# Optimization experiments

Hardware: AMD Instinct MI355X
Metric: run time of the kernel (lower is better)

Reference implementation:

```python
import jax, jax.numpy as jnp
import numpy as np
from jax import lax

B, C, T = 64, 122, 500
COUT, D, H, FF, L = 64, 128, 8, 256, 2
NSUB, NCLS = 13, 4
EPS = 1e-5


def _gelu(x):
    return jax.nn.gelu(x, approximate=False)  # torch nn.GELU default (erf)


def _bn(x, g, b, m, v):
    # eval-mode BatchNorm1d over channel dim of [N, C, T]
    scale = (g / jnp.sqrt(v + EPS))[None, :, None]
    return (x - m[None, :, None]) * scale + b[None, :, None]


def _ln(x, g, b):
    mu = x.mean(-1, keepdims=True)
    var = ((x - mu) ** 2).mean(-1, keepdims=True)
    return (x - mu) / jnp.sqrt(var + EPS) * g + b


def _conv1d(x, w, b, pad):
    y = lax.conv_general_dilated(x, w, (1,), [(pad, pad)], dimension_numbers=('NCH', 'OIH', 'NCH'))
    return y + b[None, :, None]


def forward(x, subject_ids, conv1_w, conv1_b, bn1_g, bn1_b, bn1_m, bn1_v,
            conv2_w, conv2_b, bn2_g, bn2_b, bn2_m, bn2_v,
            proj_w, proj_b, elec_emb,
            qkv_w, qkv_b, out_w, out_b, ln1_g, ln1_b,
            ff1_w, ff1_b, ff2_w, ff2_b, ln2_g, ln2_b,
            heads_w, heads_b):
    bsz = x.shape[0]
    h = x.reshape(bsz * C, 1, T)                               # [B*C, 1, T]
    h = _gelu(_bn(_conv1d(h, conv1_w, conv1_b, 4), bn1_g, bn1_b, bn1_m, bn1_v))
    h = h.reshape(bsz * C, COUT, T // 2, 2).max(-1)            # MaxPool1d(2)
    h = _gelu(_bn(_conv1d(h, conv2_w, conv2_b, 2), bn2_g, bn2_b, bn2_m, bn2_v))
    h = h.mean(-1)                                             # AdaptiveAvgPool1d(1)
    tok = h @ proj_w.T + proj_b                                # [B*C, D]
    tok = tok.reshape(bsz, C, D) + elec_emb[:, :C, :]
    dh = D // H
    inv_sqrt_dh = 1.0 / float(np.sqrt(dh))
    for l in range(L):  # post-norm TransformerEncoderLayer, gelu activation
        qkv = jnp.einsum('bsd,ed->bse', tok, qkv_w[l]) + qkv_b[l]
        q, k, v = jnp.split(qkv, 3, axis=-1)
        q = q.reshape(bsz, C, H, dh)
        k = k.reshape(bsz, C, H, dh)
        v = v.reshape(bsz, C, H, dh)
        att = jax.nn.softmax(jnp.einsum('bqhd,bkhd->bhqk', q, k) * inv_sqrt_dh, axis=-1)
        ctx = jnp.einsum('bhqk,bkhd->bqhd', att, v).reshape(bsz, C, D)
        tok = _ln(tok + ctx @ out_w[l].T + out_b[l], ln1_g[l], ln1_b[l])
        ff = _gelu(tok @ ff1_w[l].T + ff1_b[l]) @ ff2_w[l].T + ff2_b[l]
        tok = _ln(tok + ff, ln2_g[l], ln2_b[l])
    pooled = tok.mean(axis=1)                                  # [B, D]
    # per-subject head routing == gather subject's weight/bias, batched matvec
    hw = heads_w[subject_ids]                                  # [B, NCLS, D]
    hb = heads_b[subject_ids]                                  # [B, NCLS]
    return jnp.einsum('bd,bcd->bc', pooled, hw) + hb


def setup_inputs() -> dict:
    key = jax.random.key(0)
    ks = jax.random.split(key, 16)
    def n(i, shape, s=0.02):
        return jax.random.normal(ks[i], shape, jnp.float32) * s
    return {
        'x': jax.random.normal(ks[0], (B, C, T), jnp.float32),
        'subject_ids': jax.random.randint(ks[1], (B,), 0, NSUB),
        'conv1_w': n(2, (COUT, 1, 9), 0.3), 'conv1_b': jnp.zeros((COUT,), jnp.float32),
        'bn1_g': jnp.ones((COUT,), jnp.float32), 'bn1_b': jnp.zeros((COUT,), jnp.float32),
        'bn1_m': jnp.zeros((COUT,), jnp.float32), 'bn1_v': jnp.ones((COUT,), jnp.float32),
        'conv2_w': n(3, (COUT, COUT, 5), 0.05), 'conv2_b': jnp.zeros((COUT,), jnp.float32),
        'bn2_g': jnp.ones((COUT,), jnp.float32), 'bn2_b': jnp.zeros((COUT,), jnp.float32),
        'bn2_m': jnp.zeros((COUT,), jnp.float32), 'bn2_v': jnp.ones((COUT,), jnp.float32),
        'proj_w': n(4, (D, COUT), 0.05), 'proj_b': jnp.zeros((D,), jnp.float32),
        'elec_emb': n(5, (1, C, D), 0.02),
        'qkv_w': n(6, (L, 3 * D, D), 0.05), 'qkv_b': jnp.zeros((L, 3 * D), jnp.float32),
        'out_w': n(7, (L, D, D), 0.05), 'out_b': jnp.zeros((L, D), jnp.float32),
        'ln1_g': jnp.ones((L, D), jnp.float32), 'ln1_b': jnp.zeros((L, D), jnp.float32),
        'ff1_w': n(8, (L, FF, D), 0.05), 'ff1_b': jnp.zeros((L, FF), jnp.float32),
        'ff2_w': n(9, (L, D, FF), 0.05), 'ff2_b': jnp.zeros((L, D), jnp.float32),
        'ln2_g': jnp.ones((L, D), jnp.float32), 'ln2_b': jnp.zeros((L, D), jnp.float32),
        'heads_w': n(10, (NSUB, NCLS, D), 0.05), 'heads_b': jnp.zeros((NSUB, NCLS), jnp.float32),
    }


def reference(x, subject_ids, conv1_w, conv1_b, bn1_g, bn1_b, bn1_m, bn1_v,
              conv2_w, conv2_b, bn2_g, bn2_b, bn2_m, bn2_v,
              proj_w, proj_b, elec_emb,
              qkv_w, qkv_b, out_w, out_b, ln1_g, ln1_b,
              ff1_w, ff1_b, ff2_w, ff2_b, ln2_g, ln2_b,
              heads_w, heads_b):
    return forward(x, subject_ids, conv1_w, conv1_b, bn1_g, bn1_b, bn1_m, bn1_v,
                   conv2_w, conv2_b, bn2_g, bn2_b, bn2_m, bn2_v,
                   proj_w, proj_b, elec_emb,
                   qkv_w, qkv_b, out_w, out_b, ln1_g, ln1_b,
                   ff1_w, ff1_b, ff2_w, ff2_b, ln2_g, ln2_b,
                   heads_w, heads_b)
```

## Files before the change

kernel.cpp:

```cpp
#include <hip/hip_runtime.h>
#include <hip/hip_fp16.h>
#include <hip/hip_bf16.h>
#include <math.h>

#define BB 64
#define CC 122
#define TT 500
#define NCOUT 64
#define DD 128
#define HHEADS 8
#define FFDIM 256
#define NLAYER 2
#define EPS 1e-5f
#define SEQ (BB*CC)

#define WS_W2T     0u
#define WS_S1      20480u
#define WS_SH1     20544u
#define WS_S2      20608u
#define WS_SH2     20672u
#define WS_WBF     20736u
#define WS_TOK     151808u
#define WS_QKVB    1151232u
#define WS_VTB     2150656u
#define WS_GTAB    2674944u
#define WS_W1S     2675968u
#define WS_QKVB2   2676992u
#define WS_VTB2    3676416u

#define WB_QKV  0u
#define WB_OUT  98304u
#define WB_FF1  131072u
#define WB_FF2  196608u

typedef __attribute__((ext_vector_type(8))) short bf16x8;
typedef __attribute__((ext_vector_type(4))) float f32x4;

__device__ __forceinline__ unsigned short f2bf(float f) {
    unsigned int u = __float_as_uint(f);
    unsigned int r = u + 0x7FFFu + ((u >> 16) & 1u);
    return (unsigned short)(r >> 16);
}

__device__ __forceinline__ unsigned pk_bf16(float a, float b) {
    float r;
    asm("v_cvt_pk_bf16_f32 %0, %1, %2" : "=v"(r) : "v"(a), "v"(b));
    return __float_as_uint(r);
}
__device__ __forceinline__ unsigned short f2bf_hw(float f) {
    return (unsigned short)pk_bf16(f, f);
}

__device__ __forceinline__ float gelu_fast(float x) {
    float z = fabsf(x) * 0.70710678118654752f;
    float t = __builtin_amdgcn_rcpf(fmaf(0.3275911f, z, 1.0f));
    float p = fmaf(fmaf(fmaf(fmaf(1.061405429f, t, -1.453152027f), t,
                             1.421413741f), t, -0.284496736f), t, 0.254829592f);
    float e = __expf(-z * z);
    float erf_abs = fmaf(-p * t, e, 1.0f);
    float erf_x = copysignf(erf_abs, x);
    return 0.5f * x * (1.0f + erf_x);
}

__device__ __forceinline__ float gelu_idx(float p, const unsigned* __restrict__ gt) {
    p = fminf(fmaxf(p, 0.0f), 511.999f);
    int i = (int)p;
    float fr = p - (float)i;
    unsigned u = gt[i];
    __half2 h2 = *(__half2*)&u;
    float v0 = __half2float(h2.x);
    float d  = __half2float(h2.y);
    return fmaf(fr, d, v0);
}

__global__ void prep_kernel(const float* __restrict__ conv1_w, const float* __restrict__ conv1_b,
                            const float* __restrict__ bn1_g, const float* __restrict__ bn1_b,
                            const float* __restrict__ bn1_m, const float* __restrict__ bn1_v,
                            const float* __restrict__ conv2_w, const float* __restrict__ conv2_b,
                            const float* __restrict__ bn2_g, const float* __restrict__ bn2_b,
                            const float* __restrict__ bn2_m, const float* __restrict__ bn2_v,
                            const float* __restrict__ qkv_w, const float* __restrict__ out_w,
                            const float* __restrict__ ff1_w, const float* __restrict__ ff2_w,
                            float* __restrict__ ws) {
    int idx = blockIdx.x * blockDim.x + threadIdx.x;
    if (idx < 20480) {
        int ci = idx & 63; int co = (idx >> 6) & 63; int kk = idx >> 12;
        unsigned short* wt = (unsigned short*)(ws + WS_W2T);
        wt[idx] = f2bf(conv2_w[(co*64 + ci)*5 + kk]);
    } else if (idx < 20544) {
        int i = idx - 20480;
        float s = bn1_g[i] * rsqrtf(bn1_v[i] + EPS);
        ws[WS_S1 + i] = s;
        ws[WS_SH1 + i] = (conv1_b[i] - bn1_m[i]) * s + bn1_b[i];
    } else if (idx < 20608) {
        int i = idx - 20544;
        float s = bn2_g[i] * rsqrtf(bn2_v[i] + EPS);
        ws[WS_S2 + i] = s;
        ws[WS_SH2 + i] = (conv2_b[i] - bn2_m[i]) * s + bn2_b[i];
    } else if (idx < 282752) {
        int r = idx - 20608;
        unsigned short* wbf = (unsigned short*)(ws + WS_WBF);
        float v;
        if (r < 98304)       v = qkv_w[r];
        else if (r < 131072) v = out_w[r - 98304];
        else if (r < 196608) v = ff1_w[r - 131072];
        else                 v = ff2_w[r - 196608];
        wbf[r] = f2bf(v);
    } else if (idx < 283264) {
        int i = idx - 282752;
        float x0 = (i - 256) * 0.03125f;
        float x1 = x0 + 0.03125f;
        float g0 = 0.5f*x0*(1.0f + erff(x0*0.70710678118654752f));
        float g1 = 0.5f*x1*(1.0f + erff(x1*0.70710678118654752f));
        __half hv = __float2half_rn(g0);
        __half hd = __float2half_rn(g1 - g0);
        unsigned short uv = *(unsigned short*)&hv;
        unsigned short ud = *(unsigned short*)&hd;
        ((unsigned*)(ws + WS_GTAB))[i] = (unsigned)uv | ((unsigned)ud << 16);
    } else if (idx < 285312) {
        int i = idx - 283264;
        int co = i >> 5, k = i & 31;
        unsigned short* w1s = (unsigned short*)(ws + WS_W1S);
        float s = bn1_g[co] * rsqrtf(bn1_v[co] + EPS);
        w1s[i] = (k < 9) ? f2bf(conv1_w[co*9 + k] * s) : (unsigned short)0;
    }
}

__global__ __launch_bounds__(256, 4) void conv_kernel(const float* __restrict__ x,
            const float* __restrict__ proj_w, const float* __restrict__ proj_b,
            const float* __restrict__ elec,
            const float* __restrict__ wsr, float* __restrict__ tok) {
    __shared__ __align__(16) unsigned short h1s[264*64];
    __shared__ __align__(16) unsigned short xbf[544];
    __shared__ __align__(16) unsigned gtab[512];
    __shared__ float part[256];
    __shared__ float mean_l[64];
    int n = blockIdx.x;
    int c = n % CC;
    int tid = threadIdx.x;
    const float* xg = x + (size_t)n * TT;

    for (int i = tid; i < 544; i += 256) {
        unsigned short v = 0;
        if (i >= 4 && i < 504) v = f2bf_hw(xg[i-4]);
        xbf[i] = v;
    }
    if (tid < 128) {
        ((uint4*)gtab)[tid] = ((const uint4*)(wsr + WS_GTAB))[tid];
    }
    for (int idx = tid; idx < 14*64; idx += 256) {
        int rr = idx >> 6;
        int r = (rr < 2) ? rr : (rr - 2 + 252);
        h1s[r*64 + (idx & 63)] = 0;
    }
    __syncthreads();

    int lane = tid & 63;
    int w = tid >> 6;
    int ln15 = lane & 15, lg = lane >> 4;

    {
        const unsigned short* w1s = (const unsigned short*)(wsr + WS_W1S);
        bf16x8 b1f[4];
        float shp[4];
#pragma unroll
        for (int nt = 0; nt < 4; nt++) {
            int co = nt*16 + ln15;
            b1f[nt] = *(const bf16x8*)&w1s[co*32 + lg*8];
            shp[nt] = fmaf(wsr[WS_SH1 + co], 32.0f, 256.0f);
        }
        int P = w*128 + ln15*8 + lg*8;
        uint4 Va = *(const uint4*)&xbf[P];
        uint4 Vb = *(const uint4*)&xbf[P + 8];
        unsigned vwin[8] = {Va.x, Va.y, Va.z, Va.w, Vb.x, Vb.y, Vb.z, Vb.w};
#pragma unroll
        for (int a = 0; a < 4; a++) {
            union { unsigned u[4]; bf16x8 b; } Ue, Uo;
#pragma unroll
            for (int d = 0; d < 4; d++) {
                Ue.u[d] = vwin[a + d];
                Uo.u[d] = (vwin[a + d] >> 16) | (vwin[a + d + 1] << 16);
            }
            f32x4 ce[4], cod[4];
#pragma unroll
            for (int nt = 0; nt < 4; nt++) {
                ce[nt]  = __builtin_amdgcn_mfma_f32_16x16x32_bf16(Ue.b, b1f[nt],
                              (f32x4){0.f,0.f,0.f,0.f}, 0, 0, 0);
                cod[nt] = __builtin_amdgcn_mfma_f32_16x16x32_bf16(Uo.b, b1f[nt],
                              (f32x4){0.f,0.f,0.f,0.f}, 0, 0, 0);
            }
#pragma unroll
            for (int nt = 0; nt < 4; nt++) {
                int co = nt*16 + ln15;
#pragma unroll
                for (int i = 0; i < 4; i++) {
                    int tp = w*64 + lg*16 + i*4 + a;
                    if (tp < 250) {
                        float ge = gelu_idx(fmaf(ce[nt][i],  32.0f, shp[nt]), gtab);
                        float go = gelu_idx(fmaf(cod[nt][i], 32.0f, shp[nt]), gtab);
                        int r = tp + 2;
                        int cp = (co >> 3) ^ (r & 7) ^ (((r >> 4) & 1) << 1);
                        h1s[r*64 + cp*8 + (co & 7)] = f2bf_hw(fmaxf(ge, go));
                    }
                }
            }
        }
    }
    __syncthreads();

    const unsigned short* wt = (const unsigned short*)(wsr + WS_W2T);
    f32x4 acc[4][4];
#pragma unroll
    for (int mi = 0; mi < 4; mi++)
#pragma unroll
        for (int nt = 0; nt < 4; nt++) acc[mi][nt] = (f32x4){0.f, 0.f, 0.f, 0.f};

    const unsigned short* wbase = wt + ln15*64 + lg*8;
#pragma unroll
    for (int kk = 0; kk < 5; kk++) {
#pragma unroll
        for (int s = 0; s < 2; s++) {
            bf16x8 bfv[4];
#pragma unroll
            for (int nt = 0; nt < 4; nt++)
                bfv[nt] = *(const bf16x8*)(wbase + kk*4096 + nt*1024 + s*32);
#pragma unroll
            for (int mi = 0; mi < 4; mi++) {
                int r = (w*4 + mi)*16 + ln15 + kk;
                int cp = (s*4 + lg) ^ (r & 7) ^ (((r >> 4) & 1) << 1);
                bf16x8 af = *(const bf16x8*)&h1s[r*64 + cp*8];
#pragma unroll
                for (int nt = 0; nt < 4; nt++)
                    acc[mi][nt] = __builtin_amdgcn_mfma_f32_16x16x32_bf16(af, bfv[nt], acc[mi][nt], 0, 0, 0);
            }
        }
    }

#pragma unroll
    for (int nt = 0; nt < 4; nt++) {
        int co2 = nt*16 + ln15;
        float sc = wsr[WS_S2 + co2] * 32.0f;
        float sh = fmaf(wsr[WS_SH2 + co2], 32.0f, 256.0f);
        float p = 0.f;
#pragma unroll
        for (int mi = 0; mi < 4; mi++) {
            int tbase = (w*4 + mi)*16 + lg*4;
#pragma unroll
            for (int i = 0; i < 4; i++) {
                if (tbase + i < 250)
                    p += gelu_idx(fmaf(acc[mi][nt][i], sc, sh), gtab);
            }
        }
        p += __shfl_down(p, 32, 64);
        p += __shfl_down(p, 16, 64);
        if (lane < 16) part[w*64 + co2] = p;
    }
    __syncthreads();
    if (tid < 64) {
        mean_l[tid] = (part[tid] + part[64+tid] + part[128+tid] + part[192+tid]) * (1.0f/250.0f);
    }
    __syncthreads();

    if (tid < DD) {
        int d = tid;
        float a = proj_b[d] + elec[c*DD + d];
#pragma unroll 8
        for (int o = 0; o < 64; o++) a = fmaf(mean_l[o], proj_w[d*64 + o], a);
        tok[(size_t)n * DD + d] = a;
    }
}

__global__ __launch_bounds__(256) void qkv_gemm(const float* __restrict__ Aptr,
        const unsigned short* __restrict__ Bbf,
        const float* __restrict__ bias,
        unsigned short* __restrict__ qkvb,
        unsigned short* __restrict__ vtb) {
    const int tid = threadIdx.x;
    const int m0 = blockIdx.x * 32;
    const int y  = blockIdx.y;
    const int n0 = y * 128;
    __shared__ __align__(16) unsigned short As[32*128];

    const float* A = Aptr + (size_t)m0 * 128;
    for (int i = tid; i < 1024; i += 256) {
        int m = i >> 5; int kq = (i & 31)*4;
        float4 v = *(const float4*)(A + m*128 + kq);
        int cp = (kq >> 3) ^ (m & 15);
        unsigned p0 = pk_bf16(v.x, v.y);
        unsigned p1 = pk_bf16(v.z, v.w);
        *(uint2*)&As[m*128 + cp*8 + (kq & 7)] = make_uint2(p0, p1);
    }
    __syncthreads();

    const int lane = tid & 63, w = tid >> 6;
    const int ln15 = lane & 15, lg = lane >> 4;
    f32x4 acc[2][2];
#pragma unroll
    for (int mi = 0; mi < 2; mi++)
#pragma unroll
        for (int ni = 0; ni < 2; ni++) acc[mi][ni] = (f32x4){0.f, 0.f, 0.f, 0.f};

    const unsigned short* Bb = Bbf + (size_t)n0 * 128;
#pragma unroll
    for (int kt = 0; kt < 4; kt++) {
        bf16x8 af[2], bfv[2];
#pragma unroll
        for (int mi = 0; mi < 2; mi++) {
            int m = mi*16 + ln15;
            int cp = (kt*4 + lg) ^ (m & 15);
            af[mi] = *(const bf16x8*)&As[m*128 + cp*8];
        }
#pragma unroll
        for (int ni = 0; ni < 2; ni++) {
            int nn = (w*2 + ni)*16 + ln15;
            bfv[ni] = *(const bf16x8*)&Bb[(size_t)nn*128 + kt*32 + lg*8];
        }
#pragma unroll
        for (int mi = 0; mi < 2; mi++)
#pragma unroll
            for (int ni = 0; ni < 2; ni++)
                acc[mi][ni] = __builtin_amdgcn_mfma_f32_16x16x32_bf16(af[mi], bfv[ni], acc[mi][ni], 0, 0, 0);
    }

#pragma unroll
    for (int mi = 0; mi < 2; mi++)
#pragma unroll
        for (int ni = 0; ni < 2; ni++) {
            int nloc = (w*2 + ni)*16 + ln15;
            float bb = bias[n0 + nloc];
#pragma unroll
            for (int i = 0; i < 4; i++) {
                int ml = mi*16 + lg*4 + i;
                int nrow = m0 + ml;
                unsigned short us = f2bf_hw(acc[mi][ni][i] + bb);
                if (y < 2) {
                    qkvb[(size_t)nrow*256 + n0 + nloc] = us;
                } else {
                    int bq = nrow / 122;
                    int j  = nrow - bq*122;
                    vtb[((size_t)(bq*128 + nloc))*128 + j] = us;
                }
            }
        }
}

__global__ __launch_bounds__(512) void attn_tail(
        const unsigned short* __restrict__ qkvb,
        const unsigned short* __restrict__ vtb,
        const unsigned short* __restrict__ outW, const float* __restrict__ outb,
        float* __restrict__ tok,
        const float* __restrict__ ln1g, const float* __restrict__ ln1b,
        const unsigned short* __restrict__ B1, const float* __restrict__ b1,
        const unsigned short* __restrict__ B2, const float* __restrict__ b2,
        const float* __restrict__ ln2g, const float* __restrict__ ln2b,
        const unsigned short* __restrict__ Bq, const float* __restrict__ bq,
        unsigned short* __restrict__ qkvb_o, unsigned short* __restrict__ vtb_o,
        int do_qkv) {
    __shared__ float Cs[32*129];
    __shared__ __align__(16) unsigned short Pregion[8*16*128];
    __shared__ __align__(16) unsigned short ctxs[32*128];

    const int tid = threadIdx.x;
    const int blk = blockIdx.x;
    const int b = blk >> 2, mq = blk & 3;
    const int m0l = mq * 32;
    const int lane = tid & 63, w = tid >> 6;
    const int ln15 = lane & 15, lg = lane >> 4;

    const unsigned short* qb = qkvb + (size_t)b * 122 * 256;
    unsigned short* Pw = Pregion + w * 2048;

    {
        const int h = w;
#pragma unroll
        for (int mt = 0; mt < 2; mt++) {
            int mrow = m0l + mt*16 + ln15;
            int gr = (mrow < 122) ? mrow : 121;
            bf16x8 af = {0,0,0,0,0,0,0,0};
            if (lg < 2) af = *(const bf16x8*)(qb + gr*256 + h*16 + lg*8);
            f32x4 S[8];
#pragma unroll
            for (int nt = 0; nt < 8; nt++) {
                int j = nt*16 + ln15;
                int gj = (j < 122) ? j : 121;
                bf16x8 bv = {0,0,0,0,0,0,0,0};
                if (lg < 2) bv = *(const bf16x8*)(qb + gj*256 + 128 + h*16 + lg*8);
                S[nt] = __builtin_amdgcn_mfma_f32_16x16x32_bf16(af, bv,
                            (f32x4){0.f,0.f,0.f,0.f}, 0, 0, 0);
            }
            float sm[4];
#pragma unroll
            for (int i = 0; i < 4; i++) {
                float m_ = -1e30f;
#pragma unroll
                for (int nt = 0; nt < 8; nt++) {
                    float v = S[nt][i] * 0.25f;
                    if (nt == 7 && ln15 >= 10) v = -1e30f;
                    S[nt][i] = v;
                    m_ = fmaxf(m_, v);
                }
                m_ = fmaxf(m_, __shfl_xor(m_, 1, 64));
                m_ = fmaxf(m_, __shfl_xor(m_, 2, 64));
                m_ = fmaxf(m_, __shfl_xor(m_, 4, 64));
                m_ = fmaxf(m_, __shfl_xor(m_, 8, 64));
                float s_ = 0.f;
#pragma unroll
                for (int nt = 0; nt < 8; nt++) {
                    float e = __expf(S[nt][i] - m_);
                    S[nt][i] = e;
                    s_ += e;
                }
                s_ += __shfl_xor(s_, 1, 64);
                s_ += __shfl_xor(s_, 2, 64);
                s_ += __shfl_xor(s_, 4, 64);
                s_ += __shfl_xor(s_, 8, 64);
                sm[i] = s_;
            }
#pragma unroll
            for (int nt = 0; nt < 8; nt++)
#pragma unroll
                for (int i = 0; i < 4; i++) {
                    int rp = lg*4 + i;
                    int j = nt*16 + ln15;
                    int cp = (j >> 3) ^ rp;
                    Pw[rp*128 + cp*8 + (j & 7)] = f2bf_hw(S[nt][i]);
                }
            f32x4 cacc = (f32x4){0.f,0.f,0.f,0.f};
#pragma unroll
            for (int kt = 0; kt < 4; kt++) {
                bf16x8 bv = *(const bf16x8*)(vtb + ((size_t)(b*128 + h*16 + ln15))*128 + kt*32 + lg*8);
                int m = ln15;
                int cp = (kt*4 + lg) ^ m;
                bf16x8 ap = *(const bf16x8*)&Pw[m*128 + cp*8];
                cacc = __builtin_amdgcn_mfma_f32_16x16x32_bf16(ap, bv, cacc, 0, 0, 0);
            }
#pragma unroll
            for (int i = 0; i < 4; i++) {
                float inv = __builtin_amdgcn_rcpf(sm[i]);
                int rp = mt*16 + lg*4 + i;
                int ccol = h*16 + ln15;
                int cp = (ccol >> 3) ^ (rp & 15);
                ctxs[rp*128 + cp*8 + (ccol & 7)] = f2bf_hw(cacc[i] * inv);
            }
        }
    }
    __syncthreads();

    {
        f32x4 acc[2];
#pragma unroll
        for (int mi = 0; mi < 2; mi++) acc[mi] = (f32x4){0.f,0.f,0.f,0.f};
        int nn = w*16 + ln15;
#pragma unroll
        for (int kt = 0; kt < 4; kt++) {
            bf16x8 bv = *(const bf16x8*)&outW[(size_t)nn*128 + kt*32 + lg*8];
#pragma unroll
            for (int mi = 0; mi < 2; mi++) {
                int m = mi*16 + ln15;
                int cp = (kt*4 + lg) ^ (m & 15);
                bf16x8 afm = *(const bf16x8*)&ctxs[m*128 + cp*8];
                acc[mi] = __builtin_amdgcn_mfma_f32_16x16x32_bf16(afm, bv, acc[mi], 0, 0, 0);
            }
        }
        float bb = outb[nn];
#pragma unroll
        for (int mi = 0; mi < 2; mi++)
#pragma unroll
            for (int i = 0; i < 4; i++) {
                int ml = mi*16 + lg*4 + i;
                int mrow = m0l + ml;
                int grow = b*122 + ((mrow < 122) ? mrow : 121);
                Cs[ml*129 + nn] = acc[mi][i] + bb + tok[(size_t)grow*128 + nn];
            }
    }
    __syncthreads();

    unsigned short* ln1buf = Pregion;
    unsigned short* Hs = Pregion + 4096;
    {
        int r = tid >> 4, sub = tid & 15;
        float s1 = 0.f, s2 = 0.f;
#pragma unroll
        for (int j = 0; j < 8; j++) {
            float vv = Cs[r*129 + sub*8 + j];
            s1 += vv; s2 += vv*vv;
        }
        s1 += __shfl_xor(s1, 1, 64); s2 += __shfl_xor(s2, 1, 64);
        s1 += __shfl_xor(s1, 2, 64); s2 += __shfl_xor(s2, 2, 64);
        s1 += __shfl_xor(s1, 4, 64); s2 += __shfl_xor(s2, 4, 64);
        s1 += __shfl_xor(s1, 8, 64); s2 += __shfl_xor(s2, 8, 64);
        float mu = s1 * (1.0f/128.0f);
        float var = s2 * (1.0f/128.0f) - mu*mu;
        float rstd = rsqrtf(var + EPS);
#pragma unroll
        for (int j = 0; j < 8; j++) {
            int nloc = sub*8 + j;
            float vv = (Cs[r*129 + nloc] - mu) * rstd * ln1g[nloc] + ln1b[nloc];
            Cs[r*129 + nloc] = vv;
            int cp = (nloc >> 3) ^ (r & 15);
            ln1buf[r*128 + cp*8 + (nloc & 7)] = f2bf_hw(vv);
        }
    }
    __syncthreads();

    {
        f32x4 acc1[2][2];
#pragma unroll
        for (int mi = 0; mi < 2; mi++)
#pragma unroll
            for (int ni = 0; ni < 2; ni++) acc1[mi][ni] = (f32x4){0.f,0.f,0.f,0.f};
#pragma unroll
        for (int kt = 0; kt < 4; kt++) {
            bf16x8 afm[2];
#pragma unroll
            for (int mi = 0; mi < 2; mi++) {
                int m = mi*16 + ln15;
                int cp = (kt*4 + lg) ^ (m & 15);
                afm[mi] = *(const bf16x8*)&ln1buf[m*128 + cp*8];
            }
#pragma unroll
            for (int ni = 0; ni < 2; ni++) {
                int nn = (w*2 + ni)*16 + ln15;
                bf16x8 bv = *(const bf16x8*)&B1[(size_t)nn*128 + kt*32 + lg*8];
#pragma unroll
                for (int mi = 0; mi < 2; mi++)
                    acc1[mi][ni] = __builtin_amdgcn_mfma_f32_16x16x32_bf16(afm[mi], bv, acc1[mi][ni], 0, 0, 0);
            }
        }
#pragma unroll
        for (int ni = 0; ni < 2; ni++) {
            int nn = (w*2 + ni)*16 + ln15;
            float bb = b1[nn];
#pragma unroll
            for (int mi = 0; mi < 2; mi++)
#pragma unroll
                for (int i = 0; i < 4; i++) {
                    int m = mi*16 + lg*4 + i;
                    float v = gelu_fast(acc1[mi][ni][i] + bb);
                    int cp = (nn >> 3) ^ (m & 15);
                    Hs[m*256 + cp*8 + (nn & 7)] = f2bf_hw(v);
                }
        }
    }
    __syncthreads();

    {
        f32x4 acc2[2];
#pragma unroll
        for (int mi = 0; mi < 2; mi++) acc2[mi] = (f32x4){0.f,0.f,0.f,0.f};
        int nn = w*16 + ln15;
#pragma unroll
        for (int kt = 0; kt < 8; kt++) {
            bf16x8 bv = *(const bf16x8*)&B2[(size_t)nn*256 + kt*32 + lg*8];
#pragma unroll
            for (int mi = 0; mi < 2; mi++) {
                int m = mi*16 + ln15;
                int cp = (kt*4 + lg) ^ (m & 15);
                bf16x8 afm = *(const bf16x8*)&Hs[m*256 + cp*8];
                acc2[mi] = __builtin_amdgcn_mfma_f32_16x16x32_bf16(afm, bv, acc2[mi], 0, 0, 0);
            }
        }
        float bb = b2[nn];
#pragma unroll
        for (int mi = 0; mi < 2; mi++)
#pragma unroll
            for (int i = 0; i < 4; i++) {
                int ml = mi*16 + lg*4 + i;
                Cs[ml*129 + nn] = acc2[mi][i] + bb + Cs[ml*129 + nn];
            }
    }
    __syncthreads();

    {
        int r = tid >> 4, sub = tid & 15;
        float s1 = 0.f, s2 = 0.f;
#pragma unroll
        for (int j = 0; j < 8; j++) {
            float vv = Cs[r*129 + sub*8 + j];
            s1 += vv; s2 += vv*vv;
        }
        s1 += __shfl_xor(s1, 1, 64); s2 += __shfl_xor(s2, 1, 64);
        s1 += __shfl_xor(s1, 2, 64); s2 += __shfl_xor(s2, 2, 64);
        s1 += __shfl_xor(s1, 4, 64); s2 += __shfl_xor(s2, 4, 64);
        s1 += __shfl_xor(s1, 8, 64); s2 += __shfl_xor(s2, 8, 64);
        float mu = s1 * (1.0f/128.0f);
        float var = s2 * (1.0f/128.0f) - mu*mu;
        float rstd = rsqrtf(var + EPS);
        bool rowok = (m0l + r < 122);
#pragma unroll
        for (int j = 0; j < 8; j++) {
            int nloc = sub*8 + j;
            float vv = (Cs[r*129 + nloc] - mu) * rstd * ln2g[nloc] + ln2b[nloc];
            if (rowok)
                tok[((size_t)(b*122 + m0l + r))*128 + nloc] = vv;
            if (do_qkv) {
                int cp = (nloc >> 3) ^ (r & 15);
                Pregion[r*128 + cp*8 + (nloc & 7)] = f2bf_hw(vv);
            }
        }
    }

    if (do_qkv) {
        __syncthreads();
        const unsigned short* qbuf = Pregion;
        f32x4 accq[2][3];
#pragma unroll
        for (int mi = 0; mi < 2; mi++)
#pragma unroll
            for (int ni = 0; ni < 3; ni++) accq[mi][ni] = (f32x4){0.f,0.f,0.f,0.f};
#pragma unroll
        for (int kt = 0; kt < 4; kt++) {
            bf16x8 afm[2];
#pragma unroll
            for (int mi = 0; mi < 2; mi++) {
                int m = mi*16 + ln15;
                int cp = (kt*4 + lg) ^ (m & 15);
                afm[mi] = *(const bf16x8*)&qbuf[m*128 + cp*8];
            }
#pragma unroll
            for (int ni = 0; ni < 3; ni++) {
                int e = w*48 + ni*16 + ln15;
                bf16x8 bv = *(const bf16x8*)&Bq[(size_t)e*128 + kt*32 + lg*8];
#pragma unroll
                for (int mi = 0; mi < 2; mi++)
                    accq[mi][ni] = __builtin_amdgcn_mfma_f32_16x16x32_bf16(afm[mi], bv, accq[mi][ni], 0, 0, 0);
            }
        }
#pragma unroll
        for (int ni = 0; ni < 3; ni++) {
            int e = w*48 + ni*16 + ln15;
            float bb = bq[e];
#pragma unroll
            for (int mi = 0; mi < 2; mi++)
#pragma unroll
                for (int i = 0; i < 4; i++) {
                    int ml = mi*16 + lg*4 + i;
                    int mrow = m0l + ml;
                    if (mrow < 122) {
                        unsigned short us = f2bf_hw(accq[mi][ni][i] + bb);
                        int nrow = b*122 + mrow;
                        if (e < 256)
                            qkvb_o[(size_t)nrow*256 + e] = us;
                        else
                            vtb_o[((size_t)(b*128 + (e - 256)))*128 + mrow] = us;
                    }
                }
        }
    }
}

__global__ __launch_bounds__(128) void final_kernel(const float* __restrict__ tok,
        const int* __restrict__ sid,
        const float* __restrict__ hw, const float* __restrict__ hb,
        float* __restrict__ outp) {
    __shared__ float pool[DD];
    int b = blockIdx.x, tid = threadIdx.x;
    float s = 0.f;
    for (int c2 = 0; c2 < CC; c2++) s += tok[((size_t)b*CC + c2)*DD + tid];
    pool[tid] = s * (1.0f/(float)CC);
    __syncthreads();
    if (tid < 4) {
        int sb = sid[b];
        const float* w = hw + ((size_t)sb*4 + tid)*DD;
        float a = hb[sb*4 + tid];
#pragma unroll 8
        for (int d = 0; d < DD; d++) a = fmaf(pool[d], w[d], a);
        outp[b*4 + tid] = a;
    }
}

extern "C" void kernel_launch(void* const* d_in, const int* in_sizes, int n_in,
                              void* d_out, int out_size, void* d_ws, size_t ws_size,
                              hipStream_t stream) {
    const float* x       = (const float*)d_in[0];
    const int*   sid     = (const int*)  d_in[1];
    const float* conv1_w = (const float*)d_in[2];
    const float* conv1_b = (const float*)d_in[3];
    const float* bn1_g   = (const float*)d_in[4];
    const float* bn1_b   = (const float*)d_in[5];
    const float* bn1_m   = (const float*)d_in[6];
    const float* bn1_v   = (const float*)d_in[7];
    const float* conv2_w = (const float*)d_in[8];
    const float* conv2_b = (const float*)d_in[9];
    const float* bn2_g   = (const float*)d_in[10];
    const float* bn2_b   = (const float*)d_in[11];
    const float* bn2_m   = (const float*)d_in[12];
    const float* bn2_v   = (const float*)d_in[13];
    const float* proj_w  = (const float*)d_in[14];
    const float* proj_b  = (const float*)d_in[15];
    const float* elec    = (const float*)d_in[16];
    const float* qkv_w   = (const float*)d_in[17];
    const float* qkv_b   = (const float*)d_in[18];
    const float* out_w   = (const float*)d_in[19];
    const float* out_b   = (const float*)d_in[20];
    const float* ln1_g   = (const float*)d_in[21];
    const float* ln1_b   = (const float*)d_in[22];
    const float* ff1_w   = (const float*)d_in[23];
    const float* ff1_b   = (const float*)d_in[24];
    const float* ff2_w   = (const float*)d_in[25];
    const float* ff2_b   = (const float*)d_in[26];
    const float* ln2_g   = (const float*)d_in[27];
    const float* ln2_b   = (const float*)d_in[28];
    const float* heads_w = (const float*)d_in[29];
    const float* heads_b = (const float*)d_in[30];
    float* ws = (float*)d_ws;
    const unsigned short* wbf = (const unsigned short*)(ws + WS_WBF);
    unsigned short* qkvb  = (unsigned short*)(ws + WS_QKVB);
    unsigned short* vtb   = (unsigned short*)(ws + WS_VTB);
    unsigned short* qkvb2 = (unsigned short*)(ws + WS_QKVB2);
    unsigned short* vtb2  = (unsigned short*)(ws + WS_VTB2);

    prep_kernel<<<(285312 + 255)/256, 256, 0, stream>>>(
        conv1_w, conv1_b, bn1_g, bn1_b, bn1_m, bn1_v,
        conv2_w, conv2_b, bn2_g, bn2_b, bn2_m, bn2_v,
        qkv_w, out_w, ff1_w, ff2_w, ws);

    conv_kernel<<<SEQ, 256, 0, stream>>>(x, proj_w, proj_b, elec, ws, ws + WS_TOK);

    qkv_gemm<<<dim3(244,3), 256, 0, stream>>>(
        ws + WS_TOK, wbf + WB_QKV, qkv_b, qkvb, vtb);

    attn_tail<<<BB*4, 512, 0, stream>>>(
        qkvb, vtb,
        wbf + WB_OUT, out_b,
        ws + WS_TOK, ln1_g, ln1_b,
        wbf + WB_FF1, ff1_b,
        wbf + WB_FF2, ff2_b,
        ln2_g, ln2_b,
        wbf + WB_QKV + 49152, qkv_b + 384, qkvb2, vtb2, 1);

    attn_tail<<<BB*4, 512, 0, stream>>>(
        qkvb2, vtb2,
        wbf + WB_OUT + 16384, out_b + 128,
        ws + WS_TOK, ln1_g + 128, ln1_b + 128,
        wbf + WB_FF1 + 32768, ff1_b + 256,
        wbf + WB_FF2 + 32768, ff2_b + 128,
        ln2_g + 128, ln2_b + 128,
        wbf + WB_QKV, qkv_b, qkvb2, vtb2, 0);

    final_kernel<<<BB, 128, 0, stream>>>(ws + WS_TOK, sid, heads_w, heads_b, (float*)d_out);
}
```

Measured before the change: 424.8 us.

## Split conv kernel into two time halves per sequence with atomic token accumulation

Each sequence's conv stage now runs as two blocks, each covering half of the pooled time axis with a small halo. Shared memory per block and the accumulator count are halved, and launch bounds are raised so more blocks fit on each CU. The projection bias and electrode embedding are pre-written into the token buffer by the prep kernel, and each half atomically adds its partial projection. The cost is duplicated halo work, atomics on the token buffer, and a larger prep launch.

```diff
diff --git a/kernel.cpp b/kernel.cpp
--- a/kernel.cpp
+++ b/kernel.cpp
@@ -73,6 +73,10 @@
     return fmaf(fr, d, v0);
 }
 
+__device__ __forceinline__ unsigned ab16(unsigned hi, unsigned lo) {
+    return __builtin_amdgcn_alignbit(hi, lo, 16);
+}
+
 __global__ void prep_kernel(const float* __restrict__ conv1_w, const float* __restrict__ conv1_b,
                             const float* __restrict__ bn1_g, const float* __restrict__ bn1_b,
                             const float* __restrict__ bn1_m, const float* __restrict__ bn1_v,
@@ -81,6 +85,7 @@
                             const float* __restrict__ bn2_m, const float* __restrict__ bn2_v,
                             const float* __restrict__ qkv_w, const float* __restrict__ out_w,
                             const float* __restrict__ ff1_w, const float* __restrict__ ff2_w,
+                            const float* __restrict__ proj_b, const float* __restrict__ elec,
                             float* __restrict__ ws) {
     int idx = blockIdx.x * blockDim.x + threadIdx.x;
     if (idx < 20480) {
@@ -123,41 +128,47 @@
         unsigned short* w1s = (unsigned short*)(ws + WS_W1S);
         float s = bn1_g[co] * rsqrtf(bn1_v[co] + EPS);
         w1s[i] = (k < 9) ? f2bf(conv1_w[co*9 + k] * s) : (unsigned short)0;
-    }
-}
-
-__global__ __launch_bounds__(256, 4) void conv_kernel(const float* __restrict__ x,
-            const float* __restrict__ proj_w, const float* __restrict__ proj_b,
-            const float* __restrict__ elec,
+    } else if (idx < 1284736) {
+        int i = idx - 285312;
+        int d = i & 127, nn = i >> 7;
+        int cc2 = nn % CC;
+        ws[WS_TOK + i] = proj_b[d] + elec[cc2*DD + d];
+    }
+}
+
+__global__ __launch_bounds__(256, 7) void conv_kernel(const float* __restrict__ x,
+            const float* __restrict__ proj_w,
             const float* __restrict__ wsr, float* __restrict__ tok) {
-    __shared__ __align__(16) unsigned short h1s[264*64];
-    __shared__ __align__(16) unsigned short xbf[544];
+    __shared__ __align__(16) unsigned short h1l[136*64];
+    __shared__ __align__(16) unsigned short xbf[296];
     __shared__ __align__(16) unsigned gtab[512];
     __shared__ float part[256];
     __shared__ float mean_l[64];
-    int n = blockIdx.x;
-    int c = n % CC;
-    int tid = threadIdx.x;
+    const int blk = blockIdx.x;
+    const int n = blk >> 1, h = blk & 1;
+    const int tid = threadIdx.x;
+    const int XOFF = h*248 - 8;
     const float* xg = x + (size_t)n * TT;
 
-    for (int i = tid; i < 544; i += 256) {
+    for (int i = tid; i < 296; i += 256) {
+        int t = XOFF + i;
         unsigned short v = 0;
-        if (i >= 4 && i < 504) v = f2bf_hw(xg[i-4]);
+        if (t >= 0 && t < TT) v = f2bf_hw(xg[t]);
         xbf[i] = v;
     }
     if (tid < 128) {
         ((uint4*)gtab)[tid] = ((const uint4*)(wsr + WS_GTAB))[tid];
     }
-    for (int idx = tid; idx < 14*64; idx += 256) {
+    for (int idx = tid; idx < 10*64; idx += 256) {
         int rr = idx >> 6;
-        int r = (rr < 2) ? rr : (rr - 2 + 252);
-        h1s[r*64 + (idx & 63)] = 0;
-    }
-    __syncthreads();
-
-    int lane = tid & 63;
-    int w = tid >> 6;
-    int ln15 = lane & 15, lg = lane >> 4;
+        int r = (rr < 2) ? rr : (rr - 2 + 128);
+        h1l[r*64 + (idx & 63)] = 0;
+    }
+    __syncthreads();
+
+    const int lane = tid & 63;
+    const int w = tid >> 6;
+    const int ln15 = lane & 15, lg = lane >> 4;
 
     {
         const unsigned short* w1s = (const unsigned short*)(wsr + WS_W1S);
@@ -169,38 +180,40 @@
             b1f[nt] = *(const bf16x8*)&w1s[co*32 + lg*8];
             shp[nt] = fmaf(wsr[WS_SH1 + co], 32.0f, 256.0f);
         }
-        int P = w*128 + ln15*8 + lg*8;
-        uint4 Va = *(const uint4*)&xbf[P];
-        uint4 Vb = *(const uint4*)&xbf[P + 8];
-        unsigned vwin[8] = {Va.x, Va.y, Va.z, Va.w, Vb.x, Vb.y, Vb.z, Vb.w};
-#pragma unroll
-        for (int a = 0; a < 4; a++) {
+        int P = w*64 + ln15*4 + lg*8;
+        uint2 q0 = *(const uint2*)&xbf[P];
+        uint2 q1 = *(const uint2*)&xbf[P + 4];
+        uint2 q2 = *(const uint2*)&xbf[P + 8];
+        unsigned d0 = q0.x, d1 = q0.y, d2 = q1.x, d3 = q1.y, d4 = q2.x, d5 = q2.y;
+        unsigned e0 = ab16(d1,d0), e1 = ab16(d2,d1), e2 = ab16(d3,d2),
+                 e3 = ab16(d4,d3), e4 = ab16(d5,d4);
+        unsigned ev[2][4] = {{d0,d1,d2,d3},{d1,d2,d3,d4}};
+        unsigned od[2][4] = {{e0,e1,e2,e3},{e1,e2,e3,e4}};
+#pragma unroll
+        for (int a = 0; a < 2; a++) {
             union { unsigned u[4]; bf16x8 b; } Ue, Uo;
 #pragma unroll
-            for (int d = 0; d < 4; d++) {
-                Ue.u[d] = vwin[a + d];
-                Uo.u[d] = (vwin[a + d] >> 16) | (vwin[a + d + 1] << 16);
-            }
-            f32x4 ce[4], cod[4];
+            for (int d = 0; d < 4; d++) { Ue.u[d] = ev[a][d]; Uo.u[d] = od[a][d]; }
+            f32x4 ce[4], cd[4];
 #pragma unroll
             for (int nt = 0; nt < 4; nt++) {
-                ce[nt]  = __builtin_amdgcn_mfma_f32_16x16x32_bf16(Ue.b, b1f[nt],
-                              (f32x4){0.f,0.f,0.f,0.f}, 0, 0, 0);
-                cod[nt] = __builtin_amdgcn_mfma_f32_16x16x32_bf16(Uo.b, b1f[nt],
-                              (f32x4){0.f,0.f,0.f,0.f}, 0, 0, 0);
+                ce[nt] = __builtin_amdgcn_mfma_f32_16x16x32_bf16(Ue.b, b1f[nt],
+                             (f32x4){0.f,0.f,0.f,0.f}, 0, 0, 0);
+                cd[nt] = __builtin_amdgcn_mfma_f32_16x16x32_bf16(Uo.b, b1f[nt],
+                             (f32x4){0.f,0.f,0.f,0.f}, 0, 0, 0);
             }
 #pragma unroll
             for (int nt = 0; nt < 4; nt++) {
                 int co = nt*16 + ln15;
 #pragma unroll
                 for (int i = 0; i < 4; i++) {
-                    int tp = w*64 + lg*16 + i*4 + a;
-                    if (tp < 250) {
-                        float ge = gelu_idx(fmaf(ce[nt][i],  32.0f, shp[nt]), gtab);
-                        float go = gelu_idx(fmaf(cod[nt][i], 32.0f, shp[nt]), gtab);
-                        int r = tp + 2;
-                        int cp = (co >> 3) ^ (r & 7) ^ (((r >> 4) & 1) << 1);
-                        h1s[r*64 + cp*8 + (co & 7)] = f2bf_hw(fmaxf(ge, go));
+                    int tp = w*32 + (lg*4 + i)*2 + a;
+                    if (h || tp >= 2) {
+                        float ge = gelu_idx(fmaf(ce[nt][i], 32.0f, shp[nt]), gtab);
+                        float go = gelu_idx(fmaf(cd[nt][i], 32.0f, shp[nt]), gtab);
+                        int cp = (co >> 3) ^ (tp & 7) ^ (((tp >> 4) & 1) << 1)
+                                 ^ (((tp >> 5) & 1) << 2);
+                        h1l[tp*64 + cp*8 + (co & 7)] = f2bf_hw(fmaxf(ge, go));
                     }
                 }
             }
@@ -209,9 +222,9 @@
     __syncthreads();
 
     const unsigned short* wt = (const unsigned short*)(wsr + WS_W2T);
-    f32x4 acc[4][4];
-#pragma unroll
-    for (int mi = 0; mi < 4; mi++)
+    f32x4 acc[2][4];
+#pragma unroll
+    for (int mi = 0; mi < 2; mi++)
 #pragma unroll
         for (int nt = 0; nt < 4; nt++) acc[mi][nt] = (f32x4){0.f, 0.f, 0.f, 0.f};
 
@@ -225,10 +238,11 @@
             for (int nt = 0; nt < 4; nt++)
                 bfv[nt] = *(const bf16x8*)(wbase + kk*4096 + nt*1024 + s*32);
 #pragma unroll
-            for (int mi = 0; mi < 4; mi++) {
-                int r = (w*4 + mi)*16 + ln15 + kk;
-                int cp = (s*4 + lg) ^ (r & 7) ^ (((r >> 4) & 1) << 1);
-                bf16x8 af = *(const bf16x8*)&h1s[r*64 + cp*8];
+            for (int mi = 0; mi < 2; mi++) {
+                int r = (w*2 + mi)*16 + ln15 + kk;
+                int cp = (s*4 + lg) ^ (r & 7) ^ (((r >> 4) & 1) << 1)
+                         ^ (((r >> 5) & 1) << 2);
+                bf16x8 af = *(const bf16x8*)&h1l[r*64 + cp*8];
 #pragma unroll
                 for (int nt = 0; nt < 4; nt++)
                     acc[mi][nt] = __builtin_amdgcn_mfma_f32_16x16x32_bf16(af, bfv[nt], acc[mi][nt], 0, 0, 0);
@@ -236,6 +250,7 @@
         }
     }
 
+    const int NB = 124 + h*2;
 #pragma unroll
     for (int nt = 0; nt < 4; nt++) {
         int co2 = nt*16 + ln15;
@@ -243,11 +258,11 @@
         float sh = fmaf(wsr[WS_SH2 + co2], 32.0f, 256.0f);
         float p = 0.f;
 #pragma unroll
-        for (int mi = 0; mi < 4; mi++) {
-            int tbase = (w*4 + mi)*16 + lg*4;
+        for (int mi = 0; mi < 2; mi++) {
+            int obase = (w*2 + mi)*16 + lg*4;
 #pragma unroll
             for (int i = 0; i < 4; i++) {
-                if (tbase + i < 250)
+                if (obase + i < NB)
                     p += gelu_idx(fmaf(acc[mi][nt][i], sc, sh), gtab);
             }
         }
@@ -263,10 +278,10 @@
 
     if (tid < DD) {
         int d = tid;
-        float a = proj_b[d] + elec[c*DD + d];
+        float a = 0.f;
 #pragma unroll 8
         for (int o = 0; o < 64; o++) a = fmaf(mean_l[o], proj_w[d*64 + o], a);
-        tok[(size_t)n * DD + d] = a;
+        atomicAdd(&tok[(size_t)n * DD + d], a);
     }
 }
 
@@ -710,12 +725,12 @@
     unsigned short* qkvb2 = (unsigned short*)(ws + WS_QKVB2);
     unsigned short* vtb2  = (unsigned short*)(ws + WS_VTB2);
 
-    prep_kernel<<<(285312 + 255)/256, 256, 0, stream>>>(
+    prep_kernel<<<(1284736 + 255)/256, 256, 0, stream>>>(
         conv1_w, conv1_b, bn1_g, bn1_b, bn1_m, bn1_v,
         conv2_w, conv2_b, bn2_g, bn2_b, bn2_m, bn2_v,
-        qkv_w, out_w, ff1_w, ff2_w, ws);
-
-    conv_kernel<<<SEQ, 256, 0, stream>>>(x, proj_w, proj_b, elec, ws, ws + WS_TOK);
+        qkv_w, out_w, ff1_w, ff2_w, proj_b, elec, ws);
+
+    conv_kernel<<<SEQ*2, 256, 0, stream>>>(x, proj_w, ws, ws + WS_TOK);
 
     qkv_gemm<<<dim3(244,3), 256, 0, stream>>>(
         ws + WS_TOK, wbf + WB_QKV, qkv_b, qkvb, vtb);
```

Result: slower. 610.4 us (+43.7%).
